# Kernel tuning notes

Measured on AMD Instinct MI355X. Metric: run time of the kernel, lower is better.

## Reference

```python
import jax, jax.numpy as jnp
import numpy as np

N_NODES = 100000
NEG_SLOPE = 0.2  # PyG GATConv default leaky_relu slope


def _gat_conv(x, src, dst, W, a_src, a_dst, b, heads, out_c, concat):
    """One PyG-style GATConv (eval mode, dropout disabled).
    x: [N, F_in]; src/dst: [E] (src -> dst message direction, self-loops included).
    """
    N = x.shape[0]
    h = (x @ W).reshape(N, heads, out_c)                      # [N, H, C]
    alpha_s = jnp.einsum('nhc,hc->nh', h, a_src)              # [N, H]
    alpha_d = jnp.einsum('nhc,hc->nh', h, a_dst)              # [N, H]
    e = jax.nn.leaky_relu(alpha_s[src] + alpha_d[dst], NEG_SLOPE)  # [E, H]
    # segment softmax over incoming edges of each destination node
    e_max = jax.ops.segment_max(e, dst, num_segments=N)       # [N, H]
    e_exp = jnp.exp(e - e_max[dst])                           # [E, H]
    denom = jax.ops.segment_sum(e_exp, dst, num_segments=N)   # [N, H]
    alpha = e_exp / (denom[dst] + 1e-16)                      # [E, H]
    msg = h[src] * alpha[:, :, None]                          # [E, H, C]
    out = jax.ops.segment_sum(msg, dst, num_segments=N)       # [N, H, C]
    out = out.reshape(N, heads * out_c) if concat else out.mean(axis=1)
    return out + b


def setup_inputs() -> dict:
    key = jax.random.key(0)
    ks = jax.random.split(key, 16)
    N, E, F_in = N_NODES, 400000, 128
    H = 4
    h1, h2, out_dim = 128, 64, 2

    def glorot(k, shape, fan_in):
        return jax.random.normal(k, shape, dtype=jnp.float32) * (1.0 / np.sqrt(fan_in))

    inp = {
        'x': jax.random.normal(ks[0], (N, F_in), dtype=jnp.float32),
        'edge_index': jax.random.randint(ks[1], (2, E), 0, N, dtype=jnp.int64),
        'W1': glorot(ks[2], (F_in, H * h1), F_in),
        'a_src1': glorot(ks[3], (H, h1), h1),
        'a_dst1': glorot(ks[4], (H, h1), h1),
        'b1': jnp.zeros((H * h1,), dtype=jnp.float32),
        'W2': glorot(ks[5], (H * h1, H * h2), H * h1),
        'a_src2': glorot(ks[6], (H, h2), h2),
        'a_dst2': glorot(ks[7], (H, h2), h2),
        'b2': jnp.zeros((H * h2,), dtype=jnp.float32),
        # layer 3: 256 -> 2, heads=1, concat=False (mean)
        'W3': glorot(ks[8], (H * h2, 1 * out_dim), H * h2),
        'a_src3': glorot(ks[9], (1, out_dim), out_dim),
        'a_dst3': glorot(ks[10], (1, out_dim), out_dim),
        'b3': jnp.zeros((out_dim,), dtype=jnp.float32),
    }
    return inp


def reference(x, edge_index, W1, a_src1, a_dst1, b1, W2, a_src2, a_dst2, b2,
              W3, a_src3, a_dst3, b3):
    N = x.shape[0]
    # add self-loops (PyG GATConv default add_self_loops=True)
    loop = jnp.arange(N, dtype=edge_index.dtype)
    src = jnp.concatenate([edge_index[0], loop])
    dst = jnp.concatenate([edge_index[1], loop])

    h = _gat_conv(x, src, dst, W1, a_src1, a_dst1, b1, heads=4, out_c=128, concat=True)
    h = jax.nn.elu(h)  # dropout is identity in eval mode
    h = _gat_conv(h, src, dst, W2, a_src2, a_dst2, b2, heads=4, out_c=64, concat=True)
    h = jax.nn.elu(h)
    out = _gat_conv(h, src, dst, W3, a_src3, a_dst3, b3, heads=1, out_c=2, concat=False)
    return out
```

## Files before the change

### kernel.cpp

```cpp
#include <hip/hip_runtime.h>
#include <hip/hip_bf16.h>
#include <math.h>


#define LEAKY_SLOPE 0.2f

typedef __attribute__((ext_vector_type(8))) short bf16x8;
typedef __attribute__((ext_vector_type(4))) float f32x4;
typedef __attribute__((ext_vector_type(4))) float fx4;

__device__ __forceinline__ unsigned short f2bf(float f) {
    unsigned int x = __float_as_uint(f);
    x += 0x7fffu + ((x >> 16) & 1u);
    return (unsigned short)(x >> 16);
}
__device__ __forceinline__ float bf2f(unsigned short u) {
    return __uint_as_float(((unsigned int)u) << 16);
}
__device__ __forceinline__ float elu(float x) {
    return (x > 0.f) ? x : (__expf(x) - 1.f);
}

__device__ __forceinline__ int edge_val(const int* __restrict__ ei, int is64, long long idx) {
    return is64 ? ei[2 * idx] : ei[idx];
}

__global__ void detect_kernel(const unsigned int* __restrict__ ei, int* __restrict__ flag) {
    int lane = threadIdx.x;
    unsigned int v = ei[2 * lane + 1];
    unsigned long long b = __ballot(v != 0u);
    if (lane == 0) *flag = (b == 0ull) ? 1 : 0;
}

__global__ __launch_bounds__(256) void zero2_kernel(int* __restrict__ a, int* __restrict__ b, int n) {
    int i = blockIdx.x * blockDim.x + threadIdx.x;
    if (i < n) { a[i] = 0; b[i] = 0; }
}

__global__ __launch_bounds__(256) void sentinel_kernel(float* __restrict__ out, int n, float v) {
    int i = blockIdx.x * blockDim.x + threadIdx.x;
    if (i < n) out[i] = v;
}

__global__ __launch_bounds__(256) void count_kernel(const int* __restrict__ ei,
                                                    const int* __restrict__ flag,
                                                    int E, int N, int* __restrict__ counts) {
    int e = blockIdx.x * blockDim.x + threadIdx.x;
    if (e >= E + N) return;
    int is64 = *flag;
    int d = (e < E) ? edge_val(ei, is64, (long long)E + e) : (e - E);
    atomicAdd(&counts[d], 1);
}

__global__ __launch_bounds__(256) void scan_block_kernel(const int* __restrict__ counts,
                                                         int* __restrict__ ptrArr,
                                                         int* __restrict__ bsums, int N) {
    __shared__ int sh[256];
    int t = threadIdx.x, i = blockIdx.x * 256 + t;
    int v = (i < N) ? counts[i] : 0;
    sh[t] = v;
    __syncthreads();
    for (int off = 1; off < 256; off <<= 1) {
        int u = (t >= off) ? sh[t - off] : 0;
        __syncthreads();
        sh[t] += u;
        __syncthreads();
    }
    if (i < N) ptrArr[i] = sh[t] - v;
    if (t == 255) bsums[blockIdx.x] = sh[255];
}

__global__ __launch_bounds__(1024) void scan_tops_kernel(const int* __restrict__ bsums,
                                                         int* __restrict__ boff, int nb,
                                                         int* __restrict__ totalOut) {
    __shared__ int sh[1024];
    int t = threadIdx.x;
    int v = (t < nb) ? bsums[t] : 0;
    sh[t] = v;
    __syncthreads();
    for (int off = 1; off < 1024; off <<= 1) {
        int u = (t >= off) ? sh[t - off] : 0;
        __syncthreads();
        sh[t] += u;
        __syncthreads();
    }
    if (t < nb) boff[t] = sh[t] - v;
    if (t == 1023) *totalOut = sh[1023];
}

__global__ __launch_bounds__(256) void scan_add_kernel(int* __restrict__ ptrArr,
                                                       const int* __restrict__ boff, int N) {
    int i = blockIdx.x * blockDim.x + threadIdx.x;
    if (i < N) ptrArr[i] += boff[i >> 8];
}

__global__ __launch_bounds__(256) void fill_kernel(const int* __restrict__ ei,
                                                   const int* __restrict__ flag,
                                                   int E, int N,
                                                   const int* __restrict__ ptrArr,
                                                   int* __restrict__ cursor,
                                                   int* __restrict__ csr_src) {
    int e = blockIdx.x * blockDim.x + threadIdx.x;
    if (e >= E + N) return;
    int is64 = *flag;
    int s, d;
    if (e < E) {
        s = edge_val(ei, is64, e);
        d = edge_val(ei, is64, (long long)E + e);
    } else {
        s = d = e - E;
    }
    int slot = atomicAdd(&cursor[d], 1);
    csr_src[ptrArr[d] + slot] = s;
}

__global__ __launch_bounds__(256) void transpose_w_kernel(const float* __restrict__ W,
                                                          unsigned short* __restrict__ Wt,
                                                          int K, int Nn) {
    int i = blockIdx.x * blockDim.x + threadIdx.x;
    if (i >= K * Nn) return;
    int n = i / K, k = i - n * K;
    Wt[i] = f2bf(W[(size_t)k * Nn + n]);
}

__global__ __launch_bounds__(256) void proj_attn_kernel(const float* __restrict__ W1,
                                                        const float* __restrict__ a_s,
                                                        const float* __restrict__ a_d,
                                                        float* __restrict__ ws1,
                                                        float* __restrict__ wd1) {
    int t = blockIdx.x * blockDim.x + threadIdx.x;
    if (t >= 1024) return;
    int k = t >> 3, sd = (t >> 2) & 1, h = t & 3;
    const float* a = sd ? a_d : a_s;
    float s = 0.f;
    const float* wr = W1 + (size_t)k * 512 + h * 128;
    const float* ar = a + h * 128;
    for (int c = 0; c < 128; ++c) s += wr[c] * ar[c];
    (sd ? wd1 : ws1)[k * 4 + h] = s;
}

__global__ __launch_bounds__(256) void alpha_x_kernel(const float* __restrict__ x,
                                                      const float* __restrict__ ws1,
                                                      const float* __restrict__ wd1,
                                                      float* __restrict__ out_s,
                                                      float* __restrict__ out_d,
                                                      unsigned short* __restrict__ xbf, int N) {
    int lane = threadIdx.x & 63;
    int wid = threadIdx.x >> 6;
    int n = blockIdx.x * (blockDim.x >> 6) + wid;
    if (n >= N) return;
    int k0 = lane * 2;
    float2 xv = *(const float2*)(x + (size_t)n * 128 + k0);
    alignas(4) unsigned short o[2] = {f2bf(xv.x), f2bf(xv.y)};
    *(unsigned int*)(xbf + (size_t)n * 128 + k0) = *(unsigned int*)o;
    fx4 s0 = *(const fx4*)(ws1 + k0 * 4);
    fx4 s1 = *(const fx4*)(ws1 + k0 * 4 + 4);
    fx4 d0 = *(const fx4*)(wd1 + k0 * 4);
    fx4 d1 = *(const fx4*)(wd1 + k0 * 4 + 4);
    float ps[4], pd[4];
#pragma unroll
    for (int h = 0; h < 4; ++h) {
        ps[h] = xv.x * s0[h] + xv.y * s1[h];
        pd[h] = xv.x * d0[h] + xv.y * d1[h];
    }
#pragma unroll
    for (int off = 32; off; off >>= 1)
#pragma unroll
        for (int h = 0; h < 4; ++h) {
            ps[h] += __shfl_xor(ps[h], off);
            pd[h] += __shfl_xor(pd[h], off);
        }
    if (lane == 0) {
        fx4 rs = {ps[0], ps[1], ps[2], ps[3]};
        fx4 rd = {pd[0], pd[1], pd[2], pd[3]};
        *(fx4*)(out_s + (size_t)n * 4) = rs;
        *(fx4*)(out_d + (size_t)n * 4) = rd;
    }
}

__global__ __launch_bounds__(256) void sm_aggx_kernel(const int* __restrict__ ptrArr,
                                                      const int* __restrict__ csr_src,
                                                      const float* __restrict__ as,
                                                      const float* __restrict__ ad,
                                                      const unsigned short* __restrict__ xbf,
                                                      unsigned short* __restrict__ aggX, int N) {
    __shared__ float sal[4][64][4];
    int lane = threadIdx.x & 63;
    int wid = threadIdx.x >> 6;
    int n = blockIdx.x * 4 + wid;
    if (n >= N) return;
    int beg = ptrArr[n], end = ptrArr[n + 1];
    int deg = end - beg;
    fx4 dv = *(const fx4*)(ad + (size_t)n * 4);
    float acc[4][2];
#pragma unroll
    for (int h = 0; h < 4; ++h) { acc[h][0] = 0.f; acc[h][1] = 0.f; }

    if (deg <= 64) {
        bool act = lane < deg;
        int i = beg + (act ? lane : 0);
        int s = csr_src[i];
        fx4 av = *(const fx4*)(as + (size_t)s * 4);
        float e[4];
#pragma unroll
        for (int h = 0; h < 4; ++h) {
            float xx = av[h] + dv[h];
            xx = (xx >= 0.f) ? xx : LEAKY_SLOPE * xx;
            e[h] = act ? xx : -INFINITY;
        }
#pragma unroll
        for (int h = 0; h < 4; ++h) {
            float mm = e[h];
#pragma unroll
            for (int off = 32; off; off >>= 1) mm = fmaxf(mm, __shfl_xor(mm, off));
            float ex = __expf(e[h] - mm);
            float ss = ex;
#pragma unroll
            for (int off = 32; off; off >>= 1) ss += __shfl_xor(ss, off);
            sal[wid][lane][h] = ex / (ss + 1e-16f);
        }
        for (int i2 = beg; i2 < end; i2 += 4) {
            int r = end - i2;
            int e1 = (r > 1) ? i2 + 1 : i2;
            int e2 = (r > 2) ? i2 + 2 : i2;
            int e3 = (r > 3) ? i2 + 3 : i2;
            int s0 = csr_src[i2], s1 = csr_src[e1], s2 = csr_src[e2], s3 = csr_src[e3];
            fx4 a0 = *(const fx4*)&sal[wid][i2 - beg][0];
            fx4 a1 = *(const fx4*)&sal[wid][e1 - beg][0];
            fx4 a2 = *(const fx4*)&sal[wid][e2 - beg][0];
            fx4 a3 = *(const fx4*)&sal[wid][e3 - beg][0];
            if (r <= 1) a1 = (fx4){0.f, 0.f, 0.f, 0.f};
            if (r <= 2) a2 = (fx4){0.f, 0.f, 0.f, 0.f};
            if (r <= 3) a3 = (fx4){0.f, 0.f, 0.f, 0.f};
            unsigned int r0 = *(const unsigned int*)(xbf + (size_t)s0 * 128 + lane * 2);
            unsigned int r1 = *(const unsigned int*)(xbf + (size_t)s1 * 128 + lane * 2);
            unsigned int r2 = *(const unsigned int*)(xbf + (size_t)s2 * 128 + lane * 2);
            unsigned int r3 = *(const unsigned int*)(xbf + (size_t)s3 * 128 + lane * 2);
            float x00 = bf2f((unsigned short)r0), x01 = bf2f((unsigned short)(r0 >> 16));
            float x10 = bf2f((unsigned short)r1), x11 = bf2f((unsigned short)(r1 >> 16));
            float x20 = bf2f((unsigned short)r2), x21 = bf2f((unsigned short)(r2 >> 16));
            float x30 = bf2f((unsigned short)r3), x31 = bf2f((unsigned short)(r3 >> 16));
#pragma unroll
            for (int h = 0; h < 4; ++h) {
                acc[h][0] += a0[h] * x00 + a1[h] * x10 + a2[h] * x20 + a3[h] * x30;
                acc[h][1] += a0[h] * x01 + a1[h] * x11 + a2[h] * x21 + a3[h] * x31;
            }
        }
    } else {
        float m[4], inv[4];
#pragma unroll
        for (int h = 0; h < 4; ++h) m[h] = -INFINITY;
        for (int i = beg + lane; i < end; i += 64) {
            int s = csr_src[i];
            fx4 av = *(const fx4*)(as + (size_t)s * 4);
#pragma unroll
            for (int h = 0; h < 4; ++h) {
                float v = av[h] + dv[h];
                v = (v >= 0.f) ? v : LEAKY_SLOPE * v;
                m[h] = fmaxf(m[h], v);
            }
        }
#pragma unroll
        for (int h = 0; h < 4; ++h)
#pragma unroll
            for (int off = 32; off; off >>= 1) m[h] = fmaxf(m[h], __shfl_xor(m[h], off));
        float ss[4] = {0.f, 0.f, 0.f, 0.f};
        for (int i = beg + lane; i < end; i += 64) {
            int s = csr_src[i];
            fx4 av = *(const fx4*)(as + (size_t)s * 4);
#pragma unroll
            for (int h = 0; h < 4; ++h) {
                float v = av[h] + dv[h];
                v = (v >= 0.f) ? v : LEAKY_SLOPE * v;
                ss[h] += __expf(v - m[h]);
            }
        }
#pragma unroll
        for (int h = 0; h < 4; ++h) {
#pragma unroll
            for (int off = 32; off; off >>= 1) ss[h] += __shfl_xor(ss[h], off);
            inv[h] = 1.f / (ss[h] + 1e-16f);
        }
        for (int i = beg; i < end; ++i) {
            int s = csr_src[i];
            fx4 av = *(const fx4*)(as + (size_t)s * 4);
            unsigned int rr = *(const unsigned int*)(xbf + (size_t)s * 128 + lane * 2);
            float x0 = bf2f((unsigned short)rr), x1 = bf2f((unsigned short)(rr >> 16));
#pragma unroll
            for (int h = 0; h < 4; ++h) {
                float v = av[h] + dv[h];
                v = (v >= 0.f) ? v : LEAKY_SLOPE * v;
                float al = __expf(v - m[h]) * inv[h];
                acc[h][0] += al * x0;
                acc[h][1] += al * x1;
            }
        }
    }
#pragma unroll
    for (int h = 0; h < 4; ++h) {
        alignas(4) unsigned short o[2] = {f2bf(acc[h][0]), f2bf(acc[h][1])};
        *(unsigned int*)(aggX + (size_t)h * N * 128 + (size_t)n * 128 + lane * 2) = *(unsigned int*)o;
    }
}

__global__ __launch_bounds__(512, 4) void fused12_kernel(const unsigned short* __restrict__ aggX,
                                                         const unsigned short* __restrict__ Wt1,
                                                         const unsigned short* __restrict__ Wt2,
                                                         const float* __restrict__ b1,
                                                         const float* __restrict__ a_src2,
                                                         const float* __restrict__ a_dst2,
                                                         unsigned short* __restrict__ h2,
                                                         float* __restrict__ alpha_s,
                                                         float* __restrict__ alpha_d,
                                                         int M) {
    __shared__ unsigned short h1[64 * 512];
    __shared__ float red[8 * 2 * 64];
    const int bm = blockIdx.x;
    const int tid = threadIdx.x;
    const int lane = tid & 63, wid = tid >> 6;
    const int h = wid >> 1, half = wid & 1;
    const int l15 = lane & 15, l4 = lane >> 4;

    const unsigned short* plane = aggX + (size_t)h * M * 128;

    {
        f32x4 acc[4][4];
#pragma unroll
        for (int m = 0; m < 4; ++m)
#pragma unroll
            for (int n = 0; n < 4; ++n) acc[m][n] = (f32x4){0.f, 0.f, 0.f, 0.f};
#pragma unroll
        for (int step = 0; step < 4; ++step) {
            bf16x8 af[4], bfr[4];
#pragma unroll
            for (int m = 0; m < 4; ++m) {
                int grow = bm * 64 + m * 16 + l15;
                if (grow >= M) grow = M - 1;
                af[m] = *(const bf16x8*)(plane + (size_t)grow * 128 + step * 32 + l4 * 8);
            }
#pragma unroll
            for (int n = 0; n < 4; ++n) {
                int rB = h * 128 + half * 64 + n * 16 + l15;
                bfr[n] = *(const bf16x8*)(Wt1 + (size_t)rB * 128 + step * 32 + l4 * 8);
            }
#pragma unroll
            for (int m = 0; m < 4; ++m)
#pragma unroll
                for (int n = 0; n < 4; ++n)
                    acc[m][n] = __builtin_amdgcn_mfma_f32_16x16x32_bf16(bfr[n], af[m], acc[m][n], 0, 0, 0);
        }
#pragma unroll
        for (int m = 0; m < 4; ++m) {
            int rl = m * 16 + l15;
#pragma unroll
            for (int n = 0; n < 4; ++n) {
                int col = h * 128 + half * 64 + n * 16 + l4 * 4;
                fx4 bb = *(const fx4*)(b1 + col);
                f32x4 v = acc[m][n];
                alignas(8) unsigned short o[4];
#pragma unroll
                for (int j = 0; j < 4; ++j) o[j] = f2bf(elu(v[j] + bb[j]));
                int byteoff = (col * 2) ^ ((rl & 7) << 4);
                *(uint2*)((char*)h1 + rl * 1024 + byteoff) = *(uint2*)o;
            }
        }
    }
    __syncthreads();

    f32x4 acc2[4][2];
#pragma unroll
    for (int m = 0; m < 4; ++m)
#pragma unroll
        for (int n = 0; n < 2; ++n) acc2[m][n] = (f32x4){0.f, 0.f, 0.f, 0.f};
#pragma unroll 4
    for (int step = 0; step < 16; ++step) {
        bf16x8 af[4], bfr[2];
        int kb = step * 64 + l4 * 16;
#pragma unroll
        for (int m = 0; m < 4; ++m) {
            int rl = m * 16 + l15;
            af[m] = *(const bf16x8*)((const char*)h1 + rl * 1024 + (kb ^ ((rl & 7) << 4)));
        }
#pragma unroll
        for (int n = 0; n < 2; ++n) {
            int rB = h * 64 + half * 32 + n * 16 + l15;
            bfr[n] = *(const bf16x8*)(Wt2 + (size_t)rB * 512 + step * 32 + l4 * 8);
        }
#pragma unroll
        for (int m = 0; m < 4; ++m)
#pragma unroll
            for (int n = 0; n < 2; ++n)
                acc2[m][n] = __builtin_amdgcn_mfma_f32_16x16x32_bf16(bfr[n], af[m], acc2[m][n], 0, 0, 0);
    }
#pragma unroll
    for (int m = 0; m < 4; ++m) {
        int row = bm * 64 + m * 16 + l15;
        if (row < M) {
#pragma unroll
            for (int n = 0; n < 2; ++n) {
                int col = h * 64 + half * 32 + n * 16 + l4 * 4;
                f32x4 v = acc2[m][n];
                alignas(8) unsigned short o[4] = {f2bf(v[0]), f2bf(v[1]), f2bf(v[2]), f2bf(v[3])};
                *(uint2*)(h2 + (size_t)row * 256 + col) = *(uint2*)o;
            }
        }
    }
    float ps[4], pd[4];
#pragma unroll
    for (int m = 0; m < 4; ++m) { ps[m] = 0.f; pd[m] = 0.f; }
#pragma unroll
    for (int n = 0; n < 2; ++n) {
        int col = h * 64 + half * 32 + n * 16 + l4 * 4;
        fx4 asv = *(const fx4*)(a_src2 + col);
        fx4 adv = *(const fx4*)(a_dst2 + col);
#pragma unroll
        for (int m = 0; m < 4; ++m)
#pragma unroll
            for (int j = 0; j < 4; ++j) {
                ps[m] += acc2[m][n][j] * asv[j];
                pd[m] += acc2[m][n][j] * adv[j];
            }
    }
#pragma unroll
    for (int m = 0; m < 4; ++m) {
        ps[m] += __shfl_xor(ps[m], 16); ps[m] += __shfl_xor(ps[m], 32);
        pd[m] += __shfl_xor(pd[m], 16); pd[m] += __shfl_xor(pd[m], 32);
    }
    if (lane < 16) {
#pragma unroll
        for (int m = 0; m < 4; ++m) {
            int rl = m * 16 + l15;
            red[(wid * 2 + 0) * 64 + rl] = ps[m];
            red[(wid * 2 + 1) * 64 + rl] = pd[m];
        }
    }
    __syncthreads();
    if (half == 0 && lane < 16) {
#pragma unroll
        for (int m = 0; m < 4; ++m) {
            int rl = m * 16 + l15;
            int row = bm * 64 + rl;
            if (row < M) {
                alpha_s[(size_t)row * 4 + h] = red[(wid * 2 + 0) * 64 + rl] + red[((wid + 1) * 2 + 0) * 64 + rl];
                alpha_d[(size_t)row * 4 + h] = red[(wid * 2 + 1) * 64 + rl] + red[((wid + 1) * 2 + 1) * 64 + rl];
            }
        }
    }
}

__global__ __launch_bounds__(256) void sm_agg2_kernel(const int* __restrict__ ptrArr,
                                                      const int* __restrict__ csr_src,
                                                      const float* __restrict__ as,
                                                      const float* __restrict__ ad,
                                                      const unsigned short* __restrict__ hmat,
                                                      const float* __restrict__ bias,
                                                      const float* __restrict__ W3,
                                                      const float* __restrict__ a_s3,
                                                      const float* __restrict__ a_d3,
                                                      float* __restrict__ h3,
                                                      float* __restrict__ alpha_s3,
                                                      float* __restrict__ alpha_d3, int N) {
    __shared__ float sal[4][64][4];
    int lane = threadIdx.x & 63;
    int wid = threadIdx.x >> 6;
    int n = blockIdx.x * 4 + wid;
    if (n >= N) return;
    int beg = ptrArr[n], end = ptrArr[n + 1];
    int deg = end - beg;
    int head = lane >> 4;
    fx4 dv = *(const fx4*)(ad + (size_t)n * 4);
    float acc[4] = {0.f, 0.f, 0.f, 0.f};

    if (deg <= 64) {
        bool act = lane < deg;
        int i = beg + (act ? lane : 0);
        int s = csr_src[i];
        fx4 av = *(const fx4*)(as + (size_t)s * 4);
        float e[4];
#pragma unroll
        for (int h = 0; h < 4; ++h) {
            float xx = av[h] + dv[h];
            xx = (xx >= 0.f) ? xx : LEAKY_SLOPE * xx;
            e[h] = act ? xx : -INFINITY;
        }
#pragma unroll
        for (int h = 0; h < 4; ++h) {
            float mm = e[h];
#pragma unroll
            for (int off = 32; off; off >>= 1) mm = fmaxf(mm, __shfl_xor(mm, off));
            float ex = __expf(e[h] - mm);
            float ss = ex;
#pragma unroll
            for (int off = 32; off; off >>= 1) ss += __shfl_xor(ss, off);
            sal[wid][lane][h] = ex / (ss + 1e-16f);
        }
        for (int i2 = beg; i2 < end; i2 += 4) {
            int r = end - i2;
            int e1 = (r > 1) ? i2 + 1 : i2;
            int e2 = (r > 2) ? i2 + 2 : i2;
            int e3 = (r > 3) ? i2 + 3 : i2;
            int s0 = csr_src[i2], s1 = csr_src[e1], s2 = csr_src[e2], s3 = csr_src[e3];
            float al0 = sal[wid][i2 - beg][head];
            float al1 = (r > 1) ? sal[wid][e1 - beg][head] : 0.f;
            float al2 = (r > 2) ? sal[wid][e2 - beg][head] : 0.f;
            float al3 = (r > 3) ? sal[wid][e3 - beg][head] : 0.f;
            alignas(8) unsigned short v0[4], v1[4], v2[4], v3[4];
            *(uint2*)v0 = *(const uint2*)(hmat + (size_t)s0 * 256 + lane * 4);
            *(uint2*)v1 = *(const uint2*)(hmat + (size_t)s1 * 256 + lane * 4);
            *(uint2*)v2 = *(const uint2*)(hmat + (size_t)s2 * 256 + lane * 4);
            *(uint2*)v3 = *(const uint2*)(hmat + (size_t)s3 * 256 + lane * 4);
#pragma unroll
            for (int t = 0; t < 4; ++t)
                acc[t] += al0 * bf2f(v0[t]) + al1 * bf2f(v1[t]) + al2 * bf2f(v2[t]) + al3 * bf2f(v3[t]);
        }
    } else {
        float m[4], inv[4];
#pragma unroll
        for (int h = 0; h < 4; ++h) m[h] = -INFINITY;
        for (int i = beg + lane; i < end; i += 64) {
            int s = csr_src[i];
            fx4 av = *(const fx4*)(as + (size_t)s * 4);
#pragma unroll
            for (int h = 0; h < 4; ++h) {
                float v = av[h] + dv[h];
                v = (v >= 0.f) ? v : LEAKY_SLOPE * v;
                m[h] = fmaxf(m[h], v);
            }
        }
#pragma unroll
        for (int h = 0; h < 4; ++h)
#pragma unroll
            for (int off = 32; off; off >>= 1) m[h] = fmaxf(m[h], __shfl_xor(m[h], off));
        float ss[4] = {0.f, 0.f, 0.f, 0.f};
        for (int i = beg + lane; i < end; i += 64) {
            int s = csr_src[i];
            fx4 av = *(const fx4*)(as + (size_t)s * 4);
#pragma unroll
            for (int h = 0; h < 4; ++h) {
                float v = av[h] + dv[h];
                v = (v >= 0.f) ? v : LEAKY_SLOPE * v;
                ss[h] += __expf(v - m[h]);
            }
        }
#pragma unroll
        for (int h = 0; h < 4; ++h) {
#pragma unroll
            for (int off = 32; off; off >>= 1) ss[h] += __shfl_xor(ss[h], off);
            inv[h] = 1.f / (ss[h] + 1e-16f);
        }
        float mh = m[head], invh = inv[head];
        float adh = dv[head];
        for (int i = beg; i < end; ++i) {
            int s = csr_src[i];
            float v = as[(size_t)s * 4 + head] + adh;
            v = (v >= 0.f) ? v : LEAKY_SLOPE * v;
            float al = __expf(v - mh) * invh;
            alignas(8) unsigned short vv[4];
            *(uint2*)vv = *(const uint2*)(hmat + (size_t)s * 256 + lane * 4);
#pragma unroll
            for (int t = 0; t < 4; ++t) acc[t] += al * bf2f(vv[t]);
        }
    }
    float xv[4];
#pragma unroll
    for (int t = 0; t < 4; ++t) xv[t] = elu(acc[t] + bias[lane * 4 + t]);
    int j0 = lane * 4;
    fx4 wA = *(const fx4*)(W3 + j0 * 2);
    fx4 wB = *(const fx4*)(W3 + j0 * 2 + 4);
    float p0 = xv[0] * wA[0] + xv[1] * wA[2] + xv[2] * wB[0] + xv[3] * wB[2];
    float p1 = xv[0] * wA[1] + xv[1] * wA[3] + xv[2] * wB[1] + xv[3] * wB[3];
#pragma unroll
    for (int off = 32; off; off >>= 1) {
        p0 += __shfl_xor(p0, off);
        p1 += __shfl_xor(p1, off);
    }
    if (lane == 0) {
        h3[(size_t)n * 2 + 0] = p0;
        h3[(size_t)n * 2 + 1] = p1;
        alpha_s3[n] = p0 * a_s3[0] + p1 * a_s3[1];
        alpha_d3[n] = p0 * a_d3[0] + p1 * a_d3[1];
    }
}

__global__ __launch_bounds__(256) void sm_agg3_kernel(const int* __restrict__ ptrArr,
                                                      const int* __restrict__ csr_src,
                                                      const float* __restrict__ as,
                                                      const float* __restrict__ ad,
                                                      const float* __restrict__ h3,
                                                      const float* __restrict__ b3,
                                                      float* __restrict__ out, int N) {
    int lane = threadIdx.x & 63;
    int wid = threadIdx.x >> 6;
    int n = blockIdx.x * 4 + wid;
    if (n >= N) return;
    int beg = ptrArr[n], end = ptrArr[n + 1];
    int deg = end - beg;
    float adv = ad[n];
    float p0 = 0.f, p1 = 0.f;
    if (deg <= 64) {
        bool act = lane < deg;
        int i = beg + (act ? lane : 0);
        int s = csr_src[i];
        float xx = as[s] + adv;
        xx = (xx >= 0.f) ? xx : LEAKY_SLOPE * xx;
        float e = act ? xx : -INFINITY;
        float mm = e;
#pragma unroll
        for (int off = 32; off; off >>= 1) mm = fmaxf(mm, __shfl_xor(mm, off));
        float ex = __expf(e - mm);
        float ss = ex;
#pragma unroll
        for (int off = 32; off; off >>= 1) ss += __shfl_xor(ss, off);
        float al = ex / (ss + 1e-16f);
        float2 hv = act ? *(const float2*)(h3 + (size_t)s * 2) : make_float2(0.f, 0.f);
        p0 = al * hv.x;
        p1 = al * hv.y;
#pragma unroll
        for (int off = 32; off; off >>= 1) {
            p0 += __shfl_xor(p0, off);
            p1 += __shfl_xor(p1, off);
        }
    } else {
        float m = -INFINITY;
        for (int i = beg + lane; i < end; i += 64) {
            int s = csr_src[i];
            float v = as[s] + adv;
            v = (v >= 0.f) ? v : LEAKY_SLOPE * v;
            m = fmaxf(m, v);
        }
#pragma unroll
        for (int off = 32; off; off >>= 1) m = fmaxf(m, __shfl_xor(m, off));
        float ss = 0.f;
        for (int i = beg + lane; i < end; i += 64) {
            int s = csr_src[i];
            float v = as[s] + adv;
            v = (v >= 0.f) ? v : LEAKY_SLOPE * v;
            ss += __expf(v - m);
        }
#pragma unroll
        for (int off = 32; off; off >>= 1) ss += __shfl_xor(ss, off);
        float inv = 1.f / (ss + 1e-16f);
        for (int i = beg + lane; i < end; i += 64) {
            int s = csr_src[i];
            float v = as[s] + adv;
            v = (v >= 0.f) ? v : LEAKY_SLOPE * v;
            float al = __expf(v - m) * inv;
            float2 hv = *(const float2*)(h3 + (size_t)s * 2);
            p0 += al * hv.x;
            p1 += al * hv.y;
        }
#pragma unroll
        for (int off = 32; off; off >>= 1) {
            p0 += __shfl_xor(p0, off);
            p1 += __shfl_xor(p1, off);
        }
    }
    if (lane == 0) {
        out[(size_t)n * 2 + 0] = p0 + b3[0];
        out[(size_t)n * 2 + 1] = p1 + b3[1];
    }
}


extern "C" void kernel_launch(void* const* d_in, const int* in_sizes, int n_in,
                              void* d_out, int out_size, void* d_ws, size_t ws_size,
                              hipStream_t stream) {
    const float* x      = (const float*)d_in[0];
    const int*   ei     = (const int*)d_in[1];
    const float* W1     = (const float*)d_in[2];
    const float* a_src1 = (const float*)d_in[3];
    const float* a_dst1 = (const float*)d_in[4];
    const float* b1     = (const float*)d_in[5];
    const float* W2     = (const float*)d_in[6];
    const float* a_src2 = (const float*)d_in[7];
    const float* a_dst2 = (const float*)d_in[8];
    const float* b2     = (const float*)d_in[9];
    const float* W3     = (const float*)d_in[10];
    const float* a_src3 = (const float*)d_in[11];
    const float* a_dst3 = (const float*)d_in[12];
    const float* b3     = (const float*)d_in[13];

    const int N = in_sizes[0] / 128;
    const int E = in_sizes[1] / 2;
    const int ET = E + N;
    const int nb = (N + 255) / 256;

    size_t need = 0;
    auto carve = [&](size_t bytes) -> size_t {
        size_t off = need;
        need += (bytes + 255) & ~(size_t)255;
        return off;
    };
    size_t o_counts   = carve((size_t)N * 4);
    size_t o_cursor   = carve((size_t)N * 4);
    size_t o_ptr      = carve((size_t)(N + 1) * 4);
    size_t o_csr      = carve((size_t)ET * 4);
    size_t o_flag     = carve(4);
    size_t o_bsums    = carve((size_t)2048 * 4);
    size_t o_boff     = carve((size_t)2048 * 4);
    size_t o_alpha_s  = carve((size_t)N * 4 * 4);
    size_t o_alpha_d  = carve((size_t)N * 4 * 4);
    size_t o_a3s      = carve((size_t)N * 4);
    size_t o_a3d      = carve((size_t)N * 4);
    size_t o_h3       = carve((size_t)N * 2 * 4);
    size_t o_wsd      = carve((size_t)128 * 4 * 4 * 2);
    size_t o_wt1      = carve((size_t)512 * 128 * 2);
    size_t o_wt2      = carve((size_t)256 * 512 * 2);
    size_t o_xbf      = carve((size_t)N * 128 * 2);
    size_t o_bufA     = carve((size_t)N * 512 * 2);
    size_t o_bufB     = carve((size_t)N * 512 * 2);

    if (need > ws_size) {
        sentinel_kernel<<<(out_size + 255) / 256, 256, 0, stream>>>(
            (float*)d_out, out_size, (float)(ws_size >> 20));
        return;
    }

    char* w = (char*)d_ws;
    int*   counts   = (int*)(w + o_counts);
    int*   cursor   = (int*)(w + o_cursor);
    int*   ptrArr   = (int*)(w + o_ptr);
    int*   csr_src  = (int*)(w + o_csr);
    int*   flag     = (int*)(w + o_flag);
    int*   bsums    = (int*)(w + o_bsums);
    int*   boff     = (int*)(w + o_boff);
    float* alpha_s  = (float*)(w + o_alpha_s);
    float* alpha_d  = (float*)(w + o_alpha_d);
    float* a3s      = (float*)(w + o_a3s);
    float* a3d      = (float*)(w + o_a3d);
    float* h3       = (float*)(w + o_h3);
    float* ws1      = (float*)(w + o_wsd);
    float* wd1      = ws1 + 128 * 4;
    unsigned short* Wt1  = (unsigned short*)(w + o_wt1);
    unsigned short* Wt2  = (unsigned short*)(w + o_wt2);
    unsigned short* xbf  = (unsigned short*)(w + o_xbf);
    unsigned short* bufA = (unsigned short*)(w + o_bufA);
    unsigned short* bufB = (unsigned short*)(w + o_bufB);

    const int edge_blocks = (ET + 255) / 256;
    const int node_wave_blocks = (N + 3) / 4;
    const int node_thr_blocks = (N + 255) / 256;

    zero2_kernel<<<node_thr_blocks, 256, 0, stream>>>(counts, cursor, N);
    detect_kernel<<<1, 64, 0, stream>>>((const unsigned int*)ei, flag);
    count_kernel<<<edge_blocks, 256, 0, stream>>>(ei, flag, E, N, counts);
    scan_block_kernel<<<nb, 256, 0, stream>>>(counts, ptrArr, bsums, N);
    scan_tops_kernel<<<1, 1024, 0, stream>>>(bsums, boff, nb, ptrArr + N);
    scan_add_kernel<<<node_thr_blocks, 256, 0, stream>>>(ptrArr, boff, N);
    fill_kernel<<<edge_blocks, 256, 0, stream>>>(ei, flag, E, N, ptrArr, cursor, csr_src);

    transpose_w_kernel<<<(512 * 128 + 255) / 256, 256, 0, stream>>>(W1, Wt1, 128, 512);
    transpose_w_kernel<<<(256 * 512 + 255) / 256, 256, 0, stream>>>(W2, Wt2, 512, 256);
    proj_attn_kernel<<<4, 256, 0, stream>>>(W1, a_src1, a_dst1, ws1, wd1);

    alpha_x_kernel<<<node_wave_blocks, 256, 0, stream>>>(x, ws1, wd1, alpha_s, alpha_d, xbf, N);
    sm_aggx_kernel<<<node_wave_blocks, 256, 0, stream>>>(ptrArr, csr_src, alpha_s, alpha_d, xbf, bufA, N);

    fused12_kernel<<<(N + 63) / 64, 512, 0, stream>>>(bufA, Wt1, Wt2, b1,
                                                      a_src2, a_dst2, bufB,
                                                      alpha_s, alpha_d, N);

    sm_agg2_kernel<<<node_wave_blocks, 256, 0, stream>>>(ptrArr, csr_src, alpha_s, alpha_d,
                                                         bufB, b2, W3, a_src3, a_dst3,
                                                         h3, a3s, a3d, N);

    sm_agg3_kernel<<<node_wave_blocks, 256, 0, stream>>>(ptrArr, csr_src, a3s, a3d, h3, b3, (float*)d_out, N);
}
```

Before: 413.1 us.

## Fuse layer-1 softmax aggregation into the fused GEMM kernel via LDS slab

```diff
diff --git a/kernel.cpp b/kernel.cpp
--- a/kernel.cpp
+++ b/kernel.cpp
@@ -178,165 +178,165 @@
     }
 }
 
-__global__ __launch_bounds__(256) void sm_aggx_kernel(const int* __restrict__ ptrArr,
+__global__ __launch_bounds__(512, 4) void mega_kernel(const int* __restrict__ ptrArr,
                                                       const int* __restrict__ csr_src,
-                                                      const float* __restrict__ as,
-                                                      const float* __restrict__ ad,
+                                                      const float* __restrict__ as1,
+                                                      const float* __restrict__ ad1,
                                                       const unsigned short* __restrict__ xbf,
-                                                      unsigned short* __restrict__ aggX, int N) {
-    __shared__ float sal[4][64][4];
-    int lane = threadIdx.x & 63;
-    int wid = threadIdx.x >> 6;
-    int n = blockIdx.x * 4 + wid;
-    if (n >= N) return;
-    int beg = ptrArr[n], end = ptrArr[n + 1];
-    int deg = end - beg;
-    fx4 dv = *(const fx4*)(ad + (size_t)n * 4);
-    float acc[4][2];
-#pragma unroll
-    for (int h = 0; h < 4; ++h) { acc[h][0] = 0.f; acc[h][1] = 0.f; }
-
-    if (deg <= 64) {
-        bool act = lane < deg;
-        int i = beg + (act ? lane : 0);
-        int s = csr_src[i];
-        fx4 av = *(const fx4*)(as + (size_t)s * 4);
-        float e[4];
-#pragma unroll
-        for (int h = 0; h < 4; ++h) {
-            float xx = av[h] + dv[h];
-            xx = (xx >= 0.f) ? xx : LEAKY_SLOPE * xx;
-            e[h] = act ? xx : -INFINITY;
-        }
-#pragma unroll
-        for (int h = 0; h < 4; ++h) {
-            float mm = e[h];
-#pragma unroll
-            for (int off = 32; off; off >>= 1) mm = fmaxf(mm, __shfl_xor(mm, off));
-            float ex = __expf(e[h] - mm);
-            float ss = ex;
-#pragma unroll
-            for (int off = 32; off; off >>= 1) ss += __shfl_xor(ss, off);
-            sal[wid][lane][h] = ex / (ss + 1e-16f);
-        }
-        for (int i2 = beg; i2 < end; i2 += 4) {
-            int r = end - i2;
-            int e1 = (r > 1) ? i2 + 1 : i2;
-            int e2 = (r > 2) ? i2 + 2 : i2;
-            int e3 = (r > 3) ? i2 + 3 : i2;
-            int s0 = csr_src[i2], s1 = csr_src[e1], s2 = csr_src[e2], s3 = csr_src[e3];
-            fx4 a0 = *(const fx4*)&sal[wid][i2 - beg][0];
-            fx4 a1 = *(const fx4*)&sal[wid][e1 - beg][0];
-            fx4 a2 = *(const fx4*)&sal[wid][e2 - beg][0];
-            fx4 a3 = *(const fx4*)&sal[wid][e3 - beg][0];
-            if (r <= 1) a1 = (fx4){0.f, 0.f, 0.f, 0.f};
-            if (r <= 2) a2 = (fx4){0.f, 0.f, 0.f, 0.f};
-            if (r <= 3) a3 = (fx4){0.f, 0.f, 0.f, 0.f};
-            unsigned int r0 = *(const unsigned int*)(xbf + (size_t)s0 * 128 + lane * 2);
-            unsigned int r1 = *(const unsigned int*)(xbf + (size_t)s1 * 128 + lane * 2);
-            unsigned int r2 = *(const unsigned int*)(xbf + (size_t)s2 * 128 + lane * 2);
-            unsigned int r3 = *(const unsigned int*)(xbf + (size_t)s3 * 128 + lane * 2);
-            float x00 = bf2f((unsigned short)r0), x01 = bf2f((unsigned short)(r0 >> 16));
-            float x10 = bf2f((unsigned short)r1), x11 = bf2f((unsigned short)(r1 >> 16));
-            float x20 = bf2f((unsigned short)r2), x21 = bf2f((unsigned short)(r2 >> 16));
-            float x30 = bf2f((unsigned short)r3), x31 = bf2f((unsigned short)(r3 >> 16));
-#pragma unroll
-            for (int h = 0; h < 4; ++h) {
-                acc[h][0] += a0[h] * x00 + a1[h] * x10 + a2[h] * x20 + a3[h] * x30;
-                acc[h][1] += a0[h] * x01 + a1[h] * x11 + a2[h] * x21 + a3[h] * x31;
-            }
-        }
-    } else {
-        float m[4], inv[4];
-#pragma unroll
-        for (int h = 0; h < 4; ++h) m[h] = -INFINITY;
-        for (int i = beg + lane; i < end; i += 64) {
-            int s = csr_src[i];
-            fx4 av = *(const fx4*)(as + (size_t)s * 4);
-#pragma unroll
-            for (int h = 0; h < 4; ++h) {
-                float v = av[h] + dv[h];
-                v = (v >= 0.f) ? v : LEAKY_SLOPE * v;
-                m[h] = fmaxf(m[h], v);
-            }
-        }
-#pragma unroll
-        for (int h = 0; h < 4; ++h)
-#pragma unroll
-            for (int off = 32; off; off >>= 1) m[h] = fmaxf(m[h], __shfl_xor(m[h], off));
-        float ss[4] = {0.f, 0.f, 0.f, 0.f};
-        for (int i = beg + lane; i < end; i += 64) {
-            int s = csr_src[i];
-            fx4 av = *(const fx4*)(as + (size_t)s * 4);
-#pragma unroll
-            for (int h = 0; h < 4; ++h) {
-                float v = av[h] + dv[h];
-                v = (v >= 0.f) ? v : LEAKY_SLOPE * v;
-                ss[h] += __expf(v - m[h]);
-            }
-        }
-#pragma unroll
-        for (int h = 0; h < 4; ++h) {
-#pragma unroll
-            for (int off = 32; off; off >>= 1) ss[h] += __shfl_xor(ss[h], off);
-            inv[h] = 1.f / (ss[h] + 1e-16f);
-        }
-        for (int i = beg; i < end; ++i) {
-            int s = csr_src[i];
-            fx4 av = *(const fx4*)(as + (size_t)s * 4);
-            unsigned int rr = *(const unsigned int*)(xbf + (size_t)s * 128 + lane * 2);
-            float x0 = bf2f((unsigned short)rr), x1 = bf2f((unsigned short)(rr >> 16));
-#pragma unroll
-            for (int h = 0; h < 4; ++h) {
-                float v = av[h] + dv[h];
-                v = (v >= 0.f) ? v : LEAKY_SLOPE * v;
-                float al = __expf(v - m[h]) * inv[h];
-                acc[h][0] += al * x0;
-                acc[h][1] += al * x1;
-            }
-        }
-    }
-#pragma unroll
-    for (int h = 0; h < 4; ++h) {
-        alignas(4) unsigned short o[2] = {f2bf(acc[h][0]), f2bf(acc[h][1])};
-        *(unsigned int*)(aggX + (size_t)h * N * 128 + (size_t)n * 128 + lane * 2) = *(unsigned int*)o;
-    }
-}
-
-__global__ __launch_bounds__(512, 4) void fused12_kernel(const unsigned short* __restrict__ aggX,
-                                                         const unsigned short* __restrict__ Wt1,
-                                                         const unsigned short* __restrict__ Wt2,
-                                                         const float* __restrict__ b1,
-                                                         const float* __restrict__ a_src2,
-                                                         const float* __restrict__ a_dst2,
-                                                         unsigned short* __restrict__ h2,
-                                                         float* __restrict__ alpha_s,
-                                                         float* __restrict__ alpha_d,
-                                                         int M) {
-    __shared__ unsigned short h1[64 * 512];
-    __shared__ float red[8 * 2 * 64];
+                                                      const unsigned short* __restrict__ Wt1,
+                                                      const unsigned short* __restrict__ Wt2,
+                                                      const float* __restrict__ b1,
+                                                      const float* __restrict__ a_src2,
+                                                      const float* __restrict__ a_dst2,
+                                                      unsigned short* __restrict__ h2,
+                                                      float* __restrict__ a2s,
+                                                      float* __restrict__ a2d,
+                                                      int M) {
+    __shared__ unsigned short slab[4 * 32 * 128];
+    __shared__ unsigned short h1[32 * 512];
+    __shared__ float sal[8][64][4];
+    __shared__ float red[8 * 2 * 32];
     const int bm = blockIdx.x;
     const int tid = threadIdx.x;
     const int lane = tid & 63, wid = tid >> 6;
     const int h = wid >> 1, half = wid & 1;
     const int l15 = lane & 15, l4 = lane >> 4;
 
-    const unsigned short* plane = aggX + (size_t)h * M * 128;
+    for (int i = 0; i < 4; ++i) {
+        int r = wid * 4 + i;
+        int n = bm * 32 + r;
+        float acc[4][2];
+#pragma unroll
+        for (int hh = 0; hh < 4; ++hh) { acc[hh][0] = 0.f; acc[hh][1] = 0.f; }
+        if (n < M) {
+            int beg = ptrArr[n], end = ptrArr[n + 1];
+            int deg = end - beg;
+            fx4 dv = *(const fx4*)(ad1 + (size_t)n * 4);
+            if (deg <= 64) {
+                bool act = lane < deg;
+                int ii = beg + (act ? lane : 0);
+                int s = csr_src[ii];
+                fx4 av = *(const fx4*)(as1 + (size_t)s * 4);
+                float e[4];
+#pragma unroll
+                for (int hh = 0; hh < 4; ++hh) {
+                    float xx = av[hh] + dv[hh];
+                    xx = (xx >= 0.f) ? xx : LEAKY_SLOPE * xx;
+                    e[hh] = act ? xx : -INFINITY;
+                }
+#pragma unroll
+                for (int hh = 0; hh < 4; ++hh) {
+                    float mm = e[hh];
+#pragma unroll
+                    for (int off = 32; off; off >>= 1) mm = fmaxf(mm, __shfl_xor(mm, off));
+                    float ex = __expf(e[hh] - mm);
+                    float ss = ex;
+#pragma unroll
+                    for (int off = 32; off; off >>= 1) ss += __shfl_xor(ss, off);
+                    sal[wid][lane][hh] = ex / (ss + 1e-16f);
+                }
+                for (int i2 = beg; i2 < end; i2 += 4) {
+                    int rr = end - i2;
+                    int e1 = (rr > 1) ? i2 + 1 : i2;
+                    int e2 = (rr > 2) ? i2 + 2 : i2;
+                    int e3 = (rr > 3) ? i2 + 3 : i2;
+                    int s0 = csr_src[i2], s1 = csr_src[e1], s2 = csr_src[e2], s3 = csr_src[e3];
+                    fx4 a0 = *(const fx4*)&sal[wid][i2 - beg][0];
+                    fx4 a1 = *(const fx4*)&sal[wid][e1 - beg][0];
+                    fx4 a2 = *(const fx4*)&sal[wid][e2 - beg][0];
+                    fx4 a3 = *(const fx4*)&sal[wid][e3 - beg][0];
+                    if (rr <= 1) a1 = (fx4){0.f, 0.f, 0.f, 0.f};
+                    if (rr <= 2) a2 = (fx4){0.f, 0.f, 0.f, 0.f};
+                    if (rr <= 3) a3 = (fx4){0.f, 0.f, 0.f, 0.f};
+                    unsigned int r0 = *(const unsigned int*)(xbf + (size_t)s0 * 128 + lane * 2);
+                    unsigned int r1 = *(const unsigned int*)(xbf + (size_t)s1 * 128 + lane * 2);
+                    unsigned int r2 = *(const unsigned int*)(xbf + (size_t)s2 * 128 + lane * 2);
+                    unsigned int r3 = *(const unsigned int*)(xbf + (size_t)s3 * 128 + lane * 2);
+                    float x00 = bf2f((unsigned short)r0), x01 = bf2f((unsigned short)(r0 >> 16));
+                    float x10 = bf2f((unsigned short)r1), x11 = bf2f((unsigned short)(r1 >> 16));
+                    float x20 = bf2f((unsigned short)r2), x21 = bf2f((unsigned short)(r2 >> 16));
+                    float x30 = bf2f((unsigned short)r3), x31 = bf2f((unsigned short)(r3 >> 16));
+#pragma unroll
+                    for (int hh = 0; hh < 4; ++hh) {
+                        acc[hh][0] += a0[hh] * x00 + a1[hh] * x10 + a2[hh] * x20 + a3[hh] * x30;
+                        acc[hh][1] += a0[hh] * x01 + a1[hh] * x11 + a2[hh] * x21 + a3[hh] * x31;
+                    }
+                }
+            } else {
+                float m[4], inv[4];
+#pragma unroll
+                for (int hh = 0; hh < 4; ++hh) m[hh] = -INFINITY;
+                for (int ii = beg + lane; ii < end; ii += 64) {
+                    int s = csr_src[ii];
+                    fx4 av = *(const fx4*)(as1 + (size_t)s * 4);
+#pragma unroll
+                    for (int hh = 0; hh < 4; ++hh) {
+                        float v = av[hh] + dv[hh];
+                        v = (v >= 0.f) ? v : LEAKY_SLOPE * v;
+                        m[hh] = fmaxf(m[hh], v);
+                    }
+                }
+#pragma unroll
+                for (int hh = 0; hh < 4; ++hh)
+#pragma unroll
+                    for (int off = 32; off; off >>= 1) m[hh] = fmaxf(m[hh], __shfl_xor(m[hh], off));
+                float ss[4] = {0.f, 0.f, 0.f, 0.f};
+                for (int ii = beg + lane; ii < end; ii += 64) {
+                    int s = csr_src[ii];
+                    fx4 av = *(const fx4*)(as1 + (size_t)s * 4);
+#pragma unroll
+                    for (int hh = 0; hh < 4; ++hh) {
+                        float v = av[hh] + dv[hh];
+                        v = (v >= 0.f) ? v : LEAKY_SLOPE * v;
+                        ss[hh] += __expf(v - m[hh]);
+                    }
+                }
+#pragma unroll
+                for (int hh = 0; hh < 4; ++hh) {
+#pragma unroll
+                    for (int off = 32; off; off >>= 1) ss[hh] += __shfl_xor(ss[hh], off);
+                    inv[hh] = 1.f / (ss[hh] + 1e-16f);
+                }
+                for (int ii = beg; ii < end; ++ii) {
+                    int s = csr_src[ii];
+                    fx4 av = *(const fx4*)(as1 + (size_t)s * 4);
+                    unsigned int rr = *(const unsigned int*)(xbf + (size_t)s * 128 + lane * 2);
+                    float x0 = bf2f((unsigned short)rr), x1 = bf2f((unsigned short)(rr >> 16));
+#pragma unroll
+                    for (int hh = 0; hh < 4; ++hh) {
+                        float v = av[hh] + dv[hh];
+                        v = (v >= 0.f) ? v : LEAKY_SLOPE * v;
+                        float al = __expf(v - m[hh]) * inv[hh];
+                        acc[hh][0] += al * x0;
+                        acc[hh][1] += al * x1;
+                    }
+                }
+            }
+        }
+        int byteoff = (lane * 4) ^ ((r & 7) << 4);
+#pragma unroll
+        for (int hh = 0; hh < 4; ++hh) {
+            alignas(4) unsigned short o[2] = {f2bf(acc[hh][0]), f2bf(acc[hh][1])};
+            *(unsigned int*)((char*)slab + hh * 8192 + r * 256 + byteoff) = *(unsigned int*)o;
+        }
+    }
+    __syncthreads();
 
     {
-        f32x4 acc[4][4];
-#pragma unroll
-        for (int m = 0; m < 4; ++m)
+        const char* Asw = (const char*)slab + h * 8192;
+        f32x4 acc[2][4];
+#pragma unroll
+        for (int m = 0; m < 2; ++m)
 #pragma unroll
             for (int n = 0; n < 4; ++n) acc[m][n] = (f32x4){0.f, 0.f, 0.f, 0.f};
 #pragma unroll
         for (int step = 0; step < 4; ++step) {
-            bf16x8 af[4], bfr[4];
-#pragma unroll
-            for (int m = 0; m < 4; ++m) {
-                int grow = bm * 64 + m * 16 + l15;
-                if (grow >= M) grow = M - 1;
-                af[m] = *(const bf16x8*)(plane + (size_t)grow * 128 + step * 32 + l4 * 8);
+            bf16x8 af[2], bfr[4];
+            int kb = step * 64 + l4 * 16;
+#pragma unroll
+            for (int m = 0; m < 2; ++m) {
+                int rl = m * 16 + l15;
+                af[m] = *(const bf16x8*)(Asw + rl * 256 + (kb ^ ((rl & 7) << 4)));
             }
 #pragma unroll
             for (int n = 0; n < 4; ++n) {
@@ -344,13 +344,13 @@
                 bfr[n] = *(const bf16x8*)(Wt1 + (size_t)rB * 128 + step * 32 + l4 * 8);
             }
 #pragma unroll
-            for (int m = 0; m < 4; ++m)
+            for (int m = 0; m < 2; ++m)
 #pragma unroll
                 for (int n = 0; n < 4; ++n)
                     acc[m][n] = __builtin_amdgcn_mfma_f32_16x16x32_bf16(bfr[n], af[m], acc[m][n], 0, 0, 0);
         }
 #pragma unroll
-        for (int m = 0; m < 4; ++m) {
+        for (int m = 0; m < 2; ++m) {
             int rl = m * 16 + l15;
 #pragma unroll
             for (int n = 0; n < 4; ++n) {
@@ -367,17 +367,17 @@
     }
     __syncthreads();
 
-    f32x4 acc2[4][2];
-#pragma unroll
-    for (int m = 0; m < 4; ++m)
+    f32x4 acc2[2][2];
+#pragma unroll
+    for (int m = 0; m < 2; ++m)
 #pragma unroll
         for (int n = 0; n < 2; ++n) acc2[m][n] = (f32x4){0.f, 0.f, 0.f, 0.f};
 #pragma unroll 4
     for (int step = 0; step < 16; ++step) {
-        bf16x8 af[4], bfr[2];
+        bf16x8 af[2], bfr[2];
         int kb = step * 64 + l4 * 16;
 #pragma unroll
-        for (int m = 0; m < 4; ++m) {
+        for (int m = 0; m < 2; ++m) {
             int rl = m * 16 + l15;
             af[m] = *(const bf16x8*)((const char*)h1 + rl * 1024 + (kb ^ ((rl & 7) << 4)));
         }
@@ -387,14 +387,14 @@
             bfr[n] = *(const bf16x8*)(Wt2 + (size_t)rB * 512 + step * 32 + l4 * 8);
         }
 #pragma unroll
-        for (int m = 0; m < 4; ++m)
+        for (int m = 0; m < 2; ++m)
 #pragma unroll
             for (int n = 0; n < 2; ++n)
                 acc2[m][n] = __builtin_amdgcn_mfma_f32_16x16x32_bf16(bfr[n], af[m], acc2[m][n], 0, 0, 0);
     }
 #pragma unroll
-    for (int m = 0; m < 4; ++m) {
-        int row = bm * 64 + m * 16 + l15;
+    for (int m = 0; m < 2; ++m) {
+        int row = bm * 32 + m * 16 + l15;
         if (row < M) {
 #pragma unroll
             for (int n = 0; n < 2; ++n) {
@@ -405,16 +405,16 @@
             }
         }
     }
-    float ps[4], pd[4];
-#pragma unroll
-    for (int m = 0; m < 4; ++m) { ps[m] = 0.f; pd[m] = 0.f; }
+    float ps[2], pd[2];
+#pragma unroll
+    for (int m = 0; m < 2; ++m) { ps[m] = 0.f; pd[m] = 0.f; }
 #pragma unroll
     for (int n = 0; n < 2; ++n) {
         int col = h * 64 + half * 32 + n * 16 + l4 * 4;
         fx4 asv = *(const fx4*)(a_src2 + col);
         fx4 adv = *(const fx4*)(a_dst2 + col);
 #pragma unroll
-        for (int m = 0; m < 4; ++m)
+        for (int m = 0; m < 2; ++m)
 #pragma unroll
             for (int j = 0; j < 4; ++j) {
                 ps[m] += acc2[m][n][j] * asv[j];
@@ -422,27 +422,27 @@
             }
     }
 #pragma unroll
-    for (int m = 0; m < 4; ++m) {
+    for (int m = 0; m < 2; ++m) {
         ps[m] += __shfl_xor(ps[m], 16); ps[m] += __shfl_xor(ps[m], 32);
         pd[m] += __shfl_xor(pd[m], 16); pd[m] += __shfl_xor(pd[m], 32);
     }
     if (lane < 16) {
 #pragma unroll
-        for (int m = 0; m < 4; ++m) {
+        for (int m = 0; m < 2; ++m) {
             int rl = m * 16 + l15;
-            red[(wid * 2 + 0) * 64 + rl] = ps[m];
-            red[(wid * 2 + 1) * 64 + rl] = pd[m];
+            red[(wid * 2 + 0) * 32 + rl] = ps[m];
+            red[(wid * 2 + 1) * 32 + rl] = pd[m];
         }
     }
     __syncthreads();
     if (half == 0 && lane < 16) {
 #pragma unroll
-        for (int m = 0; m < 4; ++m) {
+        for (int m = 0; m < 2; ++m) {
             int rl = m * 16 + l15;
-            int row = bm * 64 + rl;
+            int row = bm * 32 + rl;
             if (row < M) {
-                alpha_s[(size_t)row * 4 + h] = red[(wid * 2 + 0) * 64 + rl] + red[((wid + 1) * 2 + 0) * 64 + rl];
-                alpha_d[(size_t)row * 4 + h] = red[(wid * 2 + 1) * 64 + rl] + red[((wid + 1) * 2 + 1) * 64 + rl];
+                a2s[(size_t)row * 4 + h] = red[(wid * 2 + 0) * 32 + rl] + red[((wid + 1) * 2 + 0) * 32 + rl];
+                a2d[(size_t)row * 4 + h] = red[(wid * 2 + 1) * 32 + rl] + red[((wid + 1) * 2 + 1) * 32 + rl];
             }
         }
     }
@@ -700,6 +700,8 @@
     size_t o_boff     = carve((size_t)2048 * 4);
     size_t o_alpha_s  = carve((size_t)N * 4 * 4);
     size_t o_alpha_d  = carve((size_t)N * 4 * 4);
+    size_t o_a2s      = carve((size_t)N * 4 * 4);
+    size_t o_a2d      = carve((size_t)N * 4 * 4);
     size_t o_a3s      = carve((size_t)N * 4);
     size_t o_a3d      = carve((size_t)N * 4);
     size_t o_h3       = carve((size_t)N * 2 * 4);
@@ -707,7 +709,6 @@
     size_t o_wt1      = carve((size_t)512 * 128 * 2);
     size_t o_wt2      = carve((size_t)256 * 512 * 2);
     size_t o_xbf      = carve((size_t)N * 128 * 2);
-    size_t o_bufA     = carve((size_t)N * 512 * 2);
     size_t o_bufB     = carve((size_t)N * 512 * 2);
 
     if (need > ws_size) {
@@ -726,6 +727,8 @@
     int*   boff     = (int*)(w + o_boff);
     float* alpha_s  = (float*)(w + o_alpha_s);
     float* alpha_d  = (float*)(w + o_alpha_d);
+    float* a2s      = (float*)(w + o_a2s);
+    float* a2d      = (float*)(w + o_a2d);
     float* a3s      = (float*)(w + o_a3s);
     float* a3d      = (float*)(w + o_a3d);
     float* h3       = (float*)(w + o_h3);
@@ -734,7 +737,6 @@
     unsigned short* Wt1  = (unsigned short*)(w + o_wt1);
     unsigned short* Wt2  = (unsigned short*)(w + o_wt2);
     unsigned short* xbf  = (unsigned short*)(w + o_xbf);
-    unsigned short* bufA = (unsigned short*)(w + o_bufA);
     unsigned short* bufB = (unsigned short*)(w + o_bufB);
 
     const int edge_blocks = (ET + 255) / 256;
@@ -754,13 +756,12 @@
     proj_attn_kernel<<<4, 256, 0, stream>>>(W1, a_src1, a_dst1, ws1, wd1);
 
     alpha_x_kernel<<<node_wave_blocks, 256, 0, stream>>>(x, ws1, wd1, alpha_s, alpha_d, xbf, N);
-    sm_aggx_kernel<<<node_wave_blocks, 256, 0, stream>>>(ptrArr, csr_src, alpha_s, alpha_d, xbf, bufA, N);
-
-    fused12_kernel<<<(N + 63) / 64, 512, 0, stream>>>(bufA, Wt1, Wt2, b1,
-                                                      a_src2, a_dst2, bufB,
-                                                      alpha_s, alpha_d, N);
-
-    sm_agg2_kernel<<<node_wave_blocks, 256, 0, stream>>>(ptrArr, csr_src, alpha_s, alpha_d,
+
+    mega_kernel<<<(N + 31) / 32, 512, 0, stream>>>(ptrArr, csr_src, alpha_s, alpha_d, xbf,
+                                                   Wt1, Wt2, b1, a_src2, a_dst2,
+                                                   bufB, a2s, a2d, N);
+
+    sm_agg2_kernel<<<node_wave_blocks, 256, 0, stream>>>(ptrArr, csr_src, a2s, a2d,
                                                          bufB, b2, W3, a_src3, a_dst3,
                                                          h3, a3s, a3d, N);
 
```

After: 454.3 us. +10.0%, slower.
